# Kernel tuning notes

Measured on AMD Instinct MI355X. Metric: run time of the kernel, lower is better.

## Reference

```python
import jax, jax.numpy as jnp
import numpy as np

K_SIZE = 5
PAD = 2  # (dilation*(k-1)+1 - stride + 1)//2 with k=5, dilation=1, stride=1
DEPTH_MAX = 192.0
SAMPLE_NUM = 15


def setup_inputs() -> dict:
    key = jax.random.key(0)
    k1, k2, k3, k4 = jax.random.split(key, 4)
    b, c, h, w = 2, 32, 256, 512
    depth = jax.random.uniform(k1, (b, 1, h, w), jnp.float32) * 100.0
    features = jax.random.normal(k2, (b, c, h, w), jnp.float32)
    guide_weight = jax.random.uniform(k3, (b, h, w, K_SIZE * K_SIZE), jnp.float32)
    sample_idx = jax.random.randint(k4, (SAMPLE_NUM,), 0, K_SIZE * K_SIZE, dtype=jnp.int32)
    return {"depth": depth, "features": features, "guide_weight": guide_weight,
            "sample_idx": sample_idx}


def _gather(xpad, rows, cols):
    # xpad [b,c,H+2p,W+2p]; rows [s,h], cols [s,w] -> [b,c,s,h,w]
    return xpad[:, :, rows[:, :, None], cols[:, None, :]]


def reference(depth, features, guide_weight, sample_idx):
    b, c, h, w = features.shape
    d = depth.reshape(b, h, w)
    valid = ((d > 0) & (d < DEPTH_MAX)).astype(features.dtype)[:, None]  # [b,1,h,w]

    # Gaussian positional weights of the sampled kernel offsets (select_index)
    ctr = K_SIZE // 2
    px = (sample_idx % K_SIZE).astype(jnp.float32)
    py = (sample_idx // K_SIZE).astype(jnp.float32)
    dis = jnp.sqrt((px - ctr) ** 2 + (py - ctr) ** 2)
    pos_w = jnp.exp(-0.5 * dis)
    pos_w = pos_w / jnp.sum(pos_w)  # [s]

    # Direct gather at sampled kernel offsets (equivalent to unfold + index_select).
    # torch Unfold kernel-position ordering is row-major: p -> (ky=p//K, kx=p%K).
    dy = sample_idx // K_SIZE
    dx = sample_idx % K_SIZE
    rows = dy[:, None] + jnp.arange(h)[None, :]  # [s,h] indices into padded image
    cols = dx[:, None] + jnp.arange(w)[None, :]  # [s,w]

    fpad = jnp.pad(features, ((0, 0), (0, 0), (PAD, PAD), (PAD, PAD)))
    vpad = jnp.pad(valid, ((0, 0), (0, 0), (PAD, PAD), (PAD, PAD)))

    sampled = _gather(fpad, rows, cols)            # [b,c,s,h,w]
    valid_s = _gather(vpad, rows, cols)[:, 0]      # [b,s,h,w]
    guide_s = jnp.take(guide_weight, sample_idx, axis=3)    # [b,h,w,s]
    guide_s = jnp.transpose(guide_s, (0, 3, 1, 2))          # [b,s,h,w]

    wgt = valid_s * pos_w[None, :, None, None] * guide_s    # use_position & use_guide
    wgt = jax.nn.softmax(wgt, axis=1)
    out = jnp.einsum('bcshw,bshw->bchw', sampled, wgt)
    return (out, features)
```

## Files before the change

### kernel.cpp

```cpp
#include <hip/hip_runtime.h>
#include <math.h>

#define K_SIZE 5
#define PAD 2
#define DEPTH_MAX 192.0f
#define S_NUM 15
#define G_NUM (K_SIZE * K_SIZE)

#define B_DIM 2
#define C_DIM 32
#define H_DIM 256
#define W_DIM 512
#define HW (H_DIM * W_DIM)
#define NPX (B_DIM * HW)

#define TX 256
#define CH_ALL 32
#define LROW 272
#define LDS_F (5 * LROW)
#define NGRP (5 * 68)
#define CTR_IDX (2 * LROW + 4)

__global__ __launch_bounds__(256) void adaptive_fused_v6(
    const float* __restrict__ depth,
    const float* __restrict__ features,
    const float* __restrict__ guide,
    const int*   __restrict__ sample_idx,
    float*       __restrict__ out)
{
    __shared__ float lds_raw[4 * 64 * G_NUM];
    float (*sbuf)[LDS_F] = reinterpret_cast<float (*)[LDS_F]>(lds_raw);

    const int t    = threadIdx.x;
    const int lane = t & 63;
    const int wid  = t >> 6;

    const int orig = blockIdx.x;
    const int lid  = (orig & 7) * 128 + (orig >> 3);
    const int tile = lid & 1;
    const int y    = (lid >> 1) & (H_DIM - 1);
    const int b    = lid >> 9;
    const int x0   = tile * TX;
    const int x    = x0 + t;

    int sidx[S_NUM];
#pragma unroll
    for (int s = 0; s < S_NUM; ++s) sidx[s] = sample_idx[s];

    {
        const int pw = b * HW + y * W_DIM + x0 + (wid << 6);
        const float* gsrc = guide + (size_t)pw * G_NUM;
        float* gw = &lds_raw[wid * 64 * G_NUM];
#pragma unroll
        for (int k = 0; k < G_NUM; ++k)
            gw[lane + 64 * k] = gsrc[lane + 64 * k];
    }
    const float* grow = &lds_raw[wid * 64 * G_NUM + lane * G_NUM];

    float posw[S_NUM];
    float psum = 0.f;
#pragma unroll
    for (int s = 0; s < S_NUM; ++s) {
        const float px = (float)(sidx[s] % K_SIZE);
        const float py = (float)(sidx[s] / K_SIZE);
        const float ddx = px - (float)(K_SIZE / 2);
        const float ddy = py - (float)(K_SIZE / 2);
        posw[s] = expf(-0.5f * sqrtf(ddx * ddx + ddy * ddy));
        psum += posw[s];
    }
    const float inv_psum = 1.f / psum;

    float raw[S_NUM];
    float inb_f[S_NUM];
    const int dbase = b * HW;
#pragma unroll
    for (int s = 0; s < S_NUM; ++s) {
        const int dy = sidx[s] / K_SIZE - PAD;
        const int dx = sidx[s] % K_SIZE - PAD;
        const int yy = y + dy;
        const int xx = x + dx;
        const bool inb = (yy >= 0) & (yy < H_DIM) & (xx >= 0) & (xx < W_DIM);
        float v = 0.f;
        if (inb) {
            const float d = depth[dbase + yy * W_DIM + xx];
            v = (d > 0.f && d < DEPTH_MAX) ? 1.f : 0.f;
        }
        raw[s]   = v * (posw[s] * inv_psum) * grow[sidx[s]];
        inb_f[s] = inb ? 1.f : 0.f;
    }

    int lidx0, lidx1 = 0;
    int soff0, soff1 = 0;
    {
        const int g   = t;
        const int row = g / 68;
        const int col = (g - row * 68) * 4;
        lidx0 = row * LROW + col;
        int ir = y + row - 2; ir = ir < 0 ? 0 : (ir > H_DIM - 1 ? H_DIM - 1 : ir);
        int ic = x0 - 4 + col; ic = ic < 0 ? 0 : (ic > W_DIM - 4 ? W_DIM - 4 : ic);
        soff0 = ir * W_DIM + ic;
    }
    const bool has2 = (t < NGRP - 256);
    if (has2) {
        const int g   = 256 + t;
        const int row = g / 68;
        const int col = (g - row * 68) * 4;
        lidx1 = row * LROW + col;
        int ir = y + row - 2; ir = ir < 0 ? 0 : (ir > H_DIM - 1 ? H_DIM - 1 : ir);
        int ic = x0 - 4 + col; ic = ic < 0 ? 0 : (ic > W_DIM - 4 ? W_DIM - 4 : ic);
        soff1 = ir * W_DIM + ic;
    }

    const size_t hw  = (size_t)HW;
    const float* fpl = features + (size_t)b * C_DIM * hw;

    float4 a0, a1, r0, r1;
    a0 = *(const float4*)(fpl + soff0);
    if (has2) a1 = *(const float4*)(fpl + soff1);
    {
        const float* f1 = fpl + hw;
        r0 = *(const float4*)(f1 + soff0);
        if (has2) r1 = *(const float4*)(f1 + soff1);
    }

    float mx = raw[0];
#pragma unroll
    for (int s = 1; s < S_NUM; ++s) mx = fmaxf(mx, raw[s]);
    float esum = 0.f;
    float wgt[S_NUM];
#pragma unroll
    for (int s = 0; s < S_NUM; ++s) {
        wgt[s] = expf(raw[s] - mx);
        esum += wgt[s];
    }
    const float inv_esum = 1.f / esum;
#pragma unroll
    for (int s = 0; s < S_NUM; ++s)
        wgt[s] = wgt[s] * inv_esum * inb_f[s];

    int ldsoff[S_NUM];
#pragma unroll
    for (int s = 0; s < S_NUM; ++s) {
        const int si = sidx[s];
        ldsoff[s] = (si / K_SIZE) * LROW + t + (si % K_SIZE) + 2;
    }

    __syncthreads();

    *(float4*)&sbuf[0][lidx0] = a0;
    if (has2) *(float4*)&sbuf[0][lidx1] = a1;
    __syncthreads();

    float* o0 = out + (size_t)b * C_DIM * hw + (size_t)y * W_DIM + x0 + t;
    float* o1 = o0 + (size_t)B_DIM * C_DIM * hw;

#pragma unroll
    for (int c = 0; c < CH_ALL; ++c) {
        if (c + 1 < CH_ALL) {
            float* dst = sbuf[(c + 1) % 3];
            *(float4*)&dst[lidx0] = r0;
            if (has2) *(float4*)&dst[lidx1] = r1;
        }
        float4 t0, t1;
        if (c + 2 < CH_ALL) {
            const float* fn = fpl + (size_t)(c + 2) * hw;
            t0 = *(const float4*)(fn + soff0);
            if (has2) t1 = *(const float4*)(fn + soff1);
        }

        const float* src = sbuf[c % 3];
        float acc = 0.f;
#pragma unroll
        for (int s = 0; s < S_NUM; ++s)
            acc = fmaf(src[ldsoff[s]], wgt[s], acc);
        const float ctr = src[CTR_IDX + t];

        o0[(size_t)c * hw] = acc;
        o1[(size_t)c * hw] = ctr;

        if (c + 2 < CH_ALL) { r0 = t0; if (has2) r1 = t1; }
        __syncthreads();
    }
}

extern "C" void kernel_launch(void* const* d_in, const int* in_sizes, int n_in,
                              void* d_out, int out_size, void* d_ws, size_t ws_size,
                              hipStream_t stream) {
    const float* depth      = (const float*)d_in[0];
    const float* features   = (const float*)d_in[1];
    const float* guide      = (const float*)d_in[2];
    const int*   sample_idx = (const int*)d_in[3];

    float* out = (float*)d_out;
    const int blocks = NPX / TX;

    adaptive_fused_v6<<<blocks, 256, 0, stream>>>(depth, features, guide,
                                                  sample_idx, out);
}
```

Before: 139.1 us.

## Shrink blocks to a single wavefront and replace block barriers with wave barriers

The tile shrinks from 256 to 64 pixels so each block is one 64-lane wavefront, and every __syncthreads becomes a wave barrier. The 5-row halo tile is 80 floats wide, so each block stages 100 float4 groups into a triple-buffered LDS ring that now fits inside the 64x25 guide buffer. The first feature-channel loads are issued earlier, before the softmax setup, to hide their latency. In exchange the halo overhead per pixel grows (80 columns for 64 outputs instead of 272 for 256), there are four times as many blocks, and correctness relies on wave-level ordering of LDS accesses.

```diff
diff --git a/kernel.cpp b/kernel.cpp
--- a/kernel.cpp
+++ b/kernel.cpp
@@ -14,32 +14,30 @@
 #define HW (H_DIM * W_DIM)
 #define NPX (B_DIM * HW)
 
-#define TX 256
+#define TX 64
 #define CH_ALL 32
-#define LROW 272
+#define LROW 80
 #define LDS_F (5 * LROW)
-#define NGRP (5 * 68)
+#define NGRP 100
 #define CTR_IDX (2 * LROW + 4)
 
-__global__ __launch_bounds__(256) void adaptive_fused_v6(
+__global__ __launch_bounds__(64, 4) void adaptive_fused_v7(
     const float* __restrict__ depth,
     const float* __restrict__ features,
     const float* __restrict__ guide,
     const int*   __restrict__ sample_idx,
     float*       __restrict__ out)
 {
-    __shared__ float lds_raw[4 * 64 * G_NUM];
+    __shared__ float lds_raw[64 * G_NUM];
     float (*sbuf)[LDS_F] = reinterpret_cast<float (*)[LDS_F]>(lds_raw);
 
-    const int t    = threadIdx.x;
-    const int lane = t & 63;
-    const int wid  = t >> 6;
+    const int t = threadIdx.x;
 
     const int orig = blockIdx.x;
-    const int lid  = (orig & 7) * 128 + (orig >> 3);
-    const int tile = lid & 1;
-    const int y    = (lid >> 1) & (H_DIM - 1);
-    const int b    = lid >> 9;
+    const int lid  = (orig & 7) * 512 + (orig >> 3);
+    const int tile = lid & 7;
+    const int y    = (lid >> 3) & (H_DIM - 1);
+    const int b    = lid >> 11;
     const int x0   = tile * TX;
     const int x    = x0 + t;
 
@@ -48,14 +46,44 @@
     for (int s = 0; s < S_NUM; ++s) sidx[s] = sample_idx[s];
 
     {
-        const int pw = b * HW + y * W_DIM + x0 + (wid << 6);
-        const float* gsrc = guide + (size_t)pw * G_NUM;
-        float* gw = &lds_raw[wid * 64 * G_NUM];
+        const float* gsrc = guide + (size_t)(b * HW + y * W_DIM + x0) * G_NUM;
 #pragma unroll
         for (int k = 0; k < G_NUM; ++k)
-            gw[lane + 64 * k] = gsrc[lane + 64 * k];
+            lds_raw[t + 64 * k] = gsrc[t + 64 * k];
     }
-    const float* grow = &lds_raw[wid * 64 * G_NUM + lane * G_NUM];
+    const float* grow = &lds_raw[t * G_NUM];
+
+    int soff0, soff1 = 0;
+    {
+        const int row = t / 20;
+        const int col = (t - row * 20) * 4;
+        int ir = y + row - 2; ir = ir < 0 ? 0 : (ir > H_DIM - 1 ? H_DIM - 1 : ir);
+        int ic = x0 - 4 + col; ic = ic < 0 ? 0 : (ic > W_DIM - 4 ? W_DIM - 4 : ic);
+        soff0 = ir * W_DIM + ic;
+    }
+    const bool has2 = (t < NGRP - 64);
+    if (has2) {
+        const int g   = 64 + t;
+        const int row = g / 20;
+        const int col = (g - row * 20) * 4;
+        int ir = y + row - 2; ir = ir < 0 ? 0 : (ir > H_DIM - 1 ? H_DIM - 1 : ir);
+        int ic = x0 - 4 + col; ic = ic < 0 ? 0 : (ic > W_DIM - 4 ? W_DIM - 4 : ic);
+        soff1 = ir * W_DIM + ic;
+    }
+    const int lidx0 = 4 * t;
+    const int lidx1 = 4 * (64 + t);
+
+    const size_t hw  = (size_t)HW;
+    const float* fpl = features + (size_t)b * C_DIM * hw;
+
+    float4 a0, a1, r0, r1;
+    a0 = *(const float4*)(fpl + soff0);
+    if (has2) a1 = *(const float4*)(fpl + soff1);
+    {
+        const float* f1 = fpl + hw;
+        r0 = *(const float4*)(f1 + soff0);
+        if (has2) r1 = *(const float4*)(f1 + soff1);
+    }
 
     float posw[S_NUM];
     float psum = 0.f;
@@ -89,40 +117,6 @@
         inb_f[s] = inb ? 1.f : 0.f;
     }
 
-    int lidx0, lidx1 = 0;
-    int soff0, soff1 = 0;
-    {
-        const int g   = t;
-        const int row = g / 68;
-        const int col = (g - row * 68) * 4;
-        lidx0 = row * LROW + col;
-        int ir = y + row - 2; ir = ir < 0 ? 0 : (ir > H_DIM - 1 ? H_DIM - 1 : ir);
-        int ic = x0 - 4 + col; ic = ic < 0 ? 0 : (ic > W_DIM - 4 ? W_DIM - 4 : ic);
-        soff0 = ir * W_DIM + ic;
-    }
-    const bool has2 = (t < NGRP - 256);
-    if (has2) {
-        const int g   = 256 + t;
-        const int row = g / 68;
-        const int col = (g - row * 68) * 4;
-        lidx1 = row * LROW + col;
-        int ir = y + row - 2; ir = ir < 0 ? 0 : (ir > H_DIM - 1 ? H_DIM - 1 : ir);
-        int ic = x0 - 4 + col; ic = ic < 0 ? 0 : (ic > W_DIM - 4 ? W_DIM - 4 : ic);
-        soff1 = ir * W_DIM + ic;
-    }
-
-    const size_t hw  = (size_t)HW;
-    const float* fpl = features + (size_t)b * C_DIM * hw;
-
-    float4 a0, a1, r0, r1;
-    a0 = *(const float4*)(fpl + soff0);
-    if (has2) a1 = *(const float4*)(fpl + soff1);
-    {
-        const float* f1 = fpl + hw;
-        r0 = *(const float4*)(f1 + soff0);
-        if (has2) r1 = *(const float4*)(f1 + soff1);
-    }
-
     float mx = raw[0];
 #pragma unroll
     for (int s = 1; s < S_NUM; ++s) mx = fmaxf(mx, raw[s]);
@@ -145,11 +139,11 @@
         ldsoff[s] = (si / K_SIZE) * LROW + t + (si % K_SIZE) + 2;
     }
 
-    __syncthreads();
+    __builtin_amdgcn_wave_barrier();
 
     *(float4*)&sbuf[0][lidx0] = a0;
     if (has2) *(float4*)&sbuf[0][lidx1] = a1;
-    __syncthreads();
+    __builtin_amdgcn_wave_barrier();
 
     float* o0 = out + (size_t)b * C_DIM * hw + (size_t)y * W_DIM + x0 + t;
     float* o1 = o0 + (size_t)B_DIM * C_DIM * hw;
@@ -167,6 +161,7 @@
             t0 = *(const float4*)(fn + soff0);
             if (has2) t1 = *(const float4*)(fn + soff1);
         }
+        __builtin_amdgcn_wave_barrier();
 
         const float* src = sbuf[c % 3];
         float acc = 0.f;
@@ -179,7 +174,7 @@
         o1[(size_t)c * hw] = ctr;
 
         if (c + 2 < CH_ALL) { r0 = t0; if (has2) r1 = t1; }
-        __syncthreads();
+        __builtin_amdgcn_wave_barrier();
     }
 }
 
@@ -194,6 +189,6 @@
     float* out = (float*)d_out;
     const int blocks = NPX / TX;
 
-    adaptive_fused_v6<<<blocks, 256, 0, stream>>>(depth, features, guide,
-                                                  sample_idx, out);
+    adaptive_fused_v7<<<blocks, 64, 0, stream>>>(depth, features, guide,
+                                                 sample_idx, out);
 }
```

Result: slower. 141.9 us (+2.1%).

## Split channels across a second grid dimension and shrink guide LDS staging

Applied to the files above, without the earlier changes.

Adds a grid y-dimension so each block handles 16 channels instead of 32, doubling block count for more parallelism and shorter per-block serial loops. The guide tile is now staged in two halves through the same LDS buffer used for feature rows, cutting LDS use to three feature-row buffers. A launch bound targets 8 blocks per CU. The cost is that each channel-half block recomputes the softmax weights and reloads depth and guide data, and the guide staging adds extra barriers.

```diff
diff --git a/kernel.cpp b/kernel.cpp
--- a/kernel.cpp
+++ b/kernel.cpp
@@ -15,25 +15,24 @@
 #define NPX (B_DIM * HW)
 
 #define TX 256
-#define CH_ALL 32
+#define CH_PER 16
 #define LROW 272
 #define LDS_F (5 * LROW)
 #define NGRP (5 * 68)
 #define CTR_IDX (2 * LROW + 4)
-
-__global__ __launch_bounds__(256) void adaptive_fused_v6(
+#define GHALF (128 * G_NUM)
+
+__global__ __launch_bounds__(256, 8) void adaptive_fused_v8(
     const float* __restrict__ depth,
     const float* __restrict__ features,
     const float* __restrict__ guide,
     const int*   __restrict__ sample_idx,
     float*       __restrict__ out)
 {
-    __shared__ float lds_raw[4 * 64 * G_NUM];
+    __shared__ float lds_raw[3 * LDS_F];
     float (*sbuf)[LDS_F] = reinterpret_cast<float (*)[LDS_F]>(lds_raw);
 
-    const int t    = threadIdx.x;
-    const int lane = t & 63;
-    const int wid  = t >> 6;
+    const int t = threadIdx.x;
 
     const int orig = blockIdx.x;
     const int lid  = (orig & 7) * 128 + (orig >> 3);
@@ -42,20 +41,45 @@
     const int b    = lid >> 9;
     const int x0   = tile * TX;
     const int x    = x0 + t;
+    const int c0   = blockIdx.y * CH_PER;
 
     int sidx[S_NUM];
 #pragma unroll
     for (int s = 0; s < S_NUM; ++s) sidx[s] = sample_idx[s];
 
+    int soff0, soff1 = 0;
+    int lidx0, lidx1 = 0;
     {
-        const int pw = b * HW + y * W_DIM + x0 + (wid << 6);
-        const float* gsrc = guide + (size_t)pw * G_NUM;
-        float* gw = &lds_raw[wid * 64 * G_NUM];
-#pragma unroll
-        for (int k = 0; k < G_NUM; ++k)
-            gw[lane + 64 * k] = gsrc[lane + 64 * k];
-    }
-    const float* grow = &lds_raw[wid * 64 * G_NUM + lane * G_NUM];
+        const int g   = t;
+        const int row = g / 68;
+        const int col = (g - row * 68) * 4;
+        lidx0 = row * LROW + col;
+        int ir = y + row - 2; ir = ir < 0 ? 0 : (ir > H_DIM - 1 ? H_DIM - 1 : ir);
+        int ic = x0 - 4 + col; ic = ic < 0 ? 0 : (ic > W_DIM - 4 ? W_DIM - 4 : ic);
+        soff0 = ir * W_DIM + ic;
+    }
+    const bool has2 = (t < NGRP - 256);
+    if (has2) {
+        const int g   = 256 + t;
+        const int row = g / 68;
+        const int col = (g - row * 68) * 4;
+        lidx1 = row * LROW + col;
+        int ir = y + row - 2; ir = ir < 0 ? 0 : (ir > H_DIM - 1 ? H_DIM - 1 : ir);
+        int ic = x0 - 4 + col; ic = ic < 0 ? 0 : (ic > W_DIM - 4 ? W_DIM - 4 : ic);
+        soff1 = ir * W_DIM + ic;
+    }
+
+    const size_t hw  = (size_t)HW;
+    const float* fpl = features + ((size_t)b * C_DIM + c0) * hw;
+
+    float4 a0, a1, r0, r1;
+    a0 = *(const float4*)(fpl + soff0);
+    if (has2) a1 = *(const float4*)(fpl + soff1);
+    {
+        const float* f1 = fpl + hw;
+        r0 = *(const float4*)(f1 + soff0);
+        if (has2) r1 = *(const float4*)(f1 + soff1);
+    }
 
     float posw[S_NUM];
     float psum = 0.f;
@@ -70,8 +94,8 @@
     }
     const float inv_psum = 1.f / psum;
 
-    float raw[S_NUM];
-    float inb_f[S_NUM];
+    float pv[S_NUM];
+    unsigned inbm = 0;
     const int dbase = b * HW;
 #pragma unroll
     for (int s = 0; s < S_NUM; ++s) {
@@ -85,42 +109,39 @@
             const float d = depth[dbase + yy * W_DIM + xx];
             v = (d > 0.f && d < DEPTH_MAX) ? 1.f : 0.f;
         }
-        raw[s]   = v * (posw[s] * inv_psum) * grow[sidx[s]];
-        inb_f[s] = inb ? 1.f : 0.f;
-    }
-
-    int lidx0, lidx1 = 0;
-    int soff0, soff1 = 0;
+        pv[s] = v * (posw[s] * inv_psum);
+        inbm |= (unsigned)inb << s;
+    }
+
+    float raw[S_NUM];
+    const float* gbase = guide + (size_t)(b * HW + y * W_DIM + x0) * G_NUM;
     {
-        const int g   = t;
-        const int row = g / 68;
-        const int col = (g - row * 68) * 4;
-        lidx0 = row * LROW + col;
-        int ir = y + row - 2; ir = ir < 0 ? 0 : (ir > H_DIM - 1 ? H_DIM - 1 : ir);
-        int ic = x0 - 4 + col; ic = ic < 0 ? 0 : (ic > W_DIM - 4 ? W_DIM - 4 : ic);
-        soff0 = ir * W_DIM + ic;
-    }
-    const bool has2 = (t < NGRP - 256);
-    if (has2) {
-        const int g   = 256 + t;
-        const int row = g / 68;
-        const int col = (g - row * 68) * 4;
-        lidx1 = row * LROW + col;
-        int ir = y + row - 2; ir = ir < 0 ? 0 : (ir > H_DIM - 1 ? H_DIM - 1 : ir);
-        int ic = x0 - 4 + col; ic = ic < 0 ? 0 : (ic > W_DIM - 4 ? W_DIM - 4 : ic);
-        soff1 = ir * W_DIM + ic;
-    }
-
-    const size_t hw  = (size_t)HW;
-    const float* fpl = features + (size_t)b * C_DIM * hw;
-
-    float4 a0, a1, r0, r1;
-    a0 = *(const float4*)(fpl + soff0);
-    if (has2) a1 = *(const float4*)(fpl + soff1);
-    {
-        const float* f1 = fpl + hw;
-        r0 = *(const float4*)(f1 + soff0);
-        if (has2) r1 = *(const float4*)(f1 + soff1);
+        const float4* gsrc = (const float4*)gbase;
+#pragma unroll
+        for (int k = 0; k < 4; ++k) {
+            const int idx = k * 256 + t;
+            if (idx < GHALF / 4) *((float4*)lds_raw + idx) = gsrc[idx];
+        }
+        __syncthreads();
+        if (t < 128) {
+            const float* gr = &lds_raw[t * G_NUM];
+#pragma unroll
+            for (int s = 0; s < S_NUM; ++s) raw[s] = pv[s] * gr[sidx[s]];
+        }
+        __syncthreads();
+        const float4* gsrc2 = (const float4*)(gbase + GHALF);
+#pragma unroll
+        for (int k = 0; k < 4; ++k) {
+            const int idx = k * 256 + t;
+            if (idx < GHALF / 4) *((float4*)lds_raw + idx) = gsrc2[idx];
+        }
+        __syncthreads();
+        if (t >= 128) {
+            const float* gr = &lds_raw[(t - 128) * G_NUM];
+#pragma unroll
+            for (int s = 0; s < S_NUM; ++s) raw[s] = pv[s] * gr[sidx[s]];
+        }
+        __syncthreads();
     }
 
     float mx = raw[0];
@@ -136,7 +157,7 @@
     const float inv_esum = 1.f / esum;
 #pragma unroll
     for (int s = 0; s < S_NUM; ++s)
-        wgt[s] = wgt[s] * inv_esum * inb_f[s];
+        wgt[s] = wgt[s] * inv_esum * (((inbm >> s) & 1u) ? 1.f : 0.f);
 
     int ldsoff[S_NUM];
 #pragma unroll
@@ -144,25 +165,23 @@
         const int si = sidx[s];
         ldsoff[s] = (si / K_SIZE) * LROW + t + (si % K_SIZE) + 2;
     }
-
-    __syncthreads();
 
     *(float4*)&sbuf[0][lidx0] = a0;
     if (has2) *(float4*)&sbuf[0][lidx1] = a1;
     __syncthreads();
 
-    float* o0 = out + (size_t)b * C_DIM * hw + (size_t)y * W_DIM + x0 + t;
+    float* o0 = out + ((size_t)b * C_DIM + c0) * hw + (size_t)y * W_DIM + x0 + t;
     float* o1 = o0 + (size_t)B_DIM * C_DIM * hw;
 
 #pragma unroll
-    for (int c = 0; c < CH_ALL; ++c) {
-        if (c + 1 < CH_ALL) {
+    for (int c = 0; c < CH_PER; ++c) {
+        if (c + 1 < CH_PER) {
             float* dst = sbuf[(c + 1) % 3];
             *(float4*)&dst[lidx0] = r0;
             if (has2) *(float4*)&dst[lidx1] = r1;
         }
         float4 t0, t1;
-        if (c + 2 < CH_ALL) {
+        if (c + 2 < CH_PER) {
             const float* fn = fpl + (size_t)(c + 2) * hw;
             t0 = *(const float4*)(fn + soff0);
             if (has2) t1 = *(const float4*)(fn + soff1);
@@ -178,7 +197,7 @@
         o0[(size_t)c * hw] = acc;
         o1[(size_t)c * hw] = ctr;
 
-        if (c + 2 < CH_ALL) { r0 = t0; if (has2) r1 = t1; }
+        if (c + 2 < CH_PER) { r0 = t0; if (has2) r1 = t1; }
         __syncthreads();
     }
 }
@@ -192,8 +211,8 @@
     const int*   sample_idx = (const int*)d_in[3];
 
     float* out = (float*)d_out;
-    const int blocks = NPX / TX;
-
-    adaptive_fused_v6<<<blocks, 256, 0, stream>>>(depth, features, guide,
-                                                  sample_idx, out);
+    dim3 grid(NPX / TX, C_DIM / CH_PER, 1);
+
+    adaptive_fused_v8<<<grid, 256, 0, stream>>>(depth, features, guide,
+                                                sample_idx, out);
 }
```

New measurement: 153.6 us. 1.1x slower.
